# Optimization experiments

Hardware: AMD Instinct MI355X
Metric: run time of the kernel (lower is better)

## Reference

```python
import jax, jax.numpy as jnp
import numpy as np

K = 3       # kernel_size
STRIDE = 1
PAD = 1
EPS = 1e-12  # F.normalize eps


def setup_inputs() -> dict:
    key = jax.random.key(0)
    k1, k2, k3 = jax.random.split(key, 3)
    x = jax.random.normal(k1, (8, 128, 112, 112), dtype=jnp.float32)
    weight = jax.random.normal(k2, (256, 128, K, K), dtype=jnp.float32)
    bias = jax.random.normal(k3, (256,), dtype=jnp.float32)
    return {"x": x, "weight": weight, "bias": bias}


def reference(x, weight, bias):
    B, C, H, W = x.shape
    Cout = weight.shape[0]
    oh = (H + 2 * PAD - K) // STRIDE + 1
    ow = (W + 2 * PAD - K) // STRIDE + 1
    # im2col: [B, C*K*K, oh, ow]; feature order (C, kh, kw), same as torch F.unfold
    patches = jax.lax.conv_general_dilated_patches(
        x, (K, K), (STRIDE, STRIDE), [(PAD, PAD), (PAD, PAD)],
        dimension_numbers=("NCHW", "OIHW", "NCHW"))
    u = patches.reshape(B, C * K * K, oh * ow)
    # L2-normalize each patch column (dim=1), matching F.normalize(p=2, dim=1)
    norm = jnp.sqrt(jnp.sum(u * u, axis=1, keepdims=True))
    u = u / jnp.maximum(norm, EPS)
    # GEMM: [Cout, C*K*K] x [B, C*K*K, L] -> [B, Cout, L]
    out = jnp.einsum("od,bdl->bol", weight.reshape(Cout, -1), u)
    out = out.reshape(B, Cout, oh, ow) + bias[None, :, None, None]
    return out
```

## Files before the change

### kernel.cpp

```cpp
#include <hip/hip_runtime.h>

#define CIN    128
#define COUT   256
#define Hh     112
#define Ww     112
#define HW     12544
#define NBATCH 8
#define NPIX   (NBATCH*HW)
#define KD     (CIN*9)
#define PH     114
#define PPIX   (NBATCH*PH*PH)

typedef __bf16         v8bf __attribute__((ext_vector_type(8)));
typedef float          v4f  __attribute__((ext_vector_type(4)));

__device__ __forceinline__ unsigned short f2bf(float f) {
  unsigned int u = __float_as_uint(f);
  u += 0x7FFFu + ((u >> 16) & 1u);
  return (unsigned short)(u >> 16);
}

__device__ __forceinline__ void gl_lds16(const void* g, void* l) {
  __builtin_amdgcn_global_load_lds(
      (const __attribute__((address_space(1))) void*)g,
      (__attribute__((address_space(3))) void*)l, 16, 0, 0);
}

#define USS 130
__global__ __launch_bounds__(256) void k_pre(
    const float* __restrict__ x, const float* __restrict__ w,
    unsigned short* __restrict__ xbp, unsigned short* __restrict__ wpk,
    float* __restrict__ sq)
{
  __shared__ unsigned short US[112 * USS];
  __shared__ float sqp[112 * 4];

  int tid = threadIdx.x;
  int bid = blockIdx.x;

  if (bid >= NBATCH * PH) {
    int t = (bid - NBATCH * PH) * 2048 + tid * 8;
#pragma unroll
    for (int i = 0; i < 8; ++i) {
      int idx = t + i;
      int o  = idx / KD;
      int rr = idx - o * KD;
      int kk = rr >> 7;
      int c  = rr & 127;
      wpk[idx] = f2bf(w[(size_t)o * KD + c * 9 + kk]);
    }
    return;
  }

  int b  = bid / PH;
  int py = bid - b * PH;
  unsigned int* dstrow = (unsigned int*)xbp +
      (size_t)(b * PH + py) * PH * (CIN / 2);

  if (py == 0 || py == PH - 1) {
    uint4 z = {0, 0, 0, 0};
    for (int h = tid; h < PH * (CIN / 8); h += 256)
      *(uint4*)(dstrow + h * 4) = z;
    return;
  }

  int oy  = py - 1;
  int l   = tid & 63;
  int wid = tid >> 6;
  const float* xp = x + (size_t)b * CIN * HW + (size_t)oy * Ww;
  bool valid = l < 56;

  float a0 = 0.0f, a1 = 0.0f;
#pragma unroll
  for (int it = 0; it < 32; ++it) {
    int c = wid * 32 + it;
    float vx = 0.0f, vy = 0.0f;
    if (valid) {
      float2 v = *(const float2*)(xp + (size_t)c * HW + 2 * l);
      vx = v.x; vy = v.y;
    }
    a0 += vx * vx;
    a1 += vy * vy;
    if (valid) {
      US[(2 * l) * USS + c]     = f2bf(vx);
      US[(2 * l + 1) * USS + c] = f2bf(vy);
    }
  }
  if (valid) { sqp[(2 * l) * 4 + wid] = a0; sqp[(2 * l + 1) * 4 + wid] = a1; }
  __syncthreads();

  if (tid < 112) {
    float s = sqp[tid * 4] + sqp[tid * 4 + 1] + sqp[tid * 4 + 2] + sqp[tid * 4 + 3];
    sq[(size_t)b * HW + (size_t)oy * Ww + tid] = s;
  }

  unsigned int* dst = dstrow + (CIN / 2);
  for (int h = tid; h < 112 * 16; h += 256) {
    int px = h >> 4, part = h & 15;
    const unsigned short* s = &US[px * USS + part * 8];
    uint4 vv;
    vv.x = *(const unsigned int*)(s + 0);
    vv.y = *(const unsigned int*)(s + 2);
    vv.z = *(const unsigned int*)(s + 4);
    vv.w = *(const unsigned int*)(s + 6);
    *(uint4*)(dst + h * 4) = vv;
  }

  if (tid < 32) {
    uint4 z = {0, 0, 0, 0};
    int px   = (tid >> 4) ? (PH - 1) : 0;
    int part = tid & 15;
    *(uint4*)(dstrow + px * (CIN / 2) + part * 4) = z;
  }
}

__device__ __forceinline__ void conv_tile(
    unsigned short* Ab, unsigned short* Bb,
    int t, bool do_stage,
    v4f (&acc)[8][4], const int (&pb)[4],
    const unsigned short* __restrict__ asrc,
    const unsigned short* __restrict__ xbp,
    int wm, int wn, int quad, int l16, int wid)
{
#pragma unroll
  for (int h = 0; h < 2; ++h) {
    v8bf bfr[4];
    int cch = (h * 4 + quad) ^ (l16 & 7);
#pragma unroll
    for (int nt = 0; nt < 4; ++nt)
      bfr[nt] = *(const v8bf*)&Bb[(wn * 64 + nt * 16 + l16) * 64 + cch * 8];
#pragma unroll
    for (int mh = 0; mh < 2; ++mh) {
      v8bf af[4];
#pragma unroll
      for (int m2 = 0; m2 < 4; ++m2)
        af[m2] = *(const v8bf*)&Ab[(wm * 128 + (mh * 4 + m2) * 16 + l16) * 64 + cch * 8];
      __builtin_amdgcn_s_setprio(1);
#pragma unroll
      for (int m2 = 0; m2 < 4; ++m2)
#pragma unroll
        for (int nt = 0; nt < 4; ++nt)
          acc[mh * 4 + m2][nt] = __builtin_amdgcn_mfma_f32_16x16x32_bf16(
              af[m2], bfr[nt], acc[mh * 4 + m2][nt], 0, 0, 0);
      __builtin_amdgcn_s_setprio(0);
    }
  }
  __builtin_amdgcn_sched_barrier(0);
  __builtin_amdgcn_s_barrier();
  __builtin_amdgcn_sched_barrier(0);
  if (do_stage) {
    int t2 = t + 2;
    int kk = t2 >> 1;
    int kh = kk / 3, kw = kk - 3 * kh;
    int soff = (kh * PH + kw) * CIN + (t2 & 1) * 64;
#pragma unroll
    for (int jj = 0; jj < 4; ++jj)
      gl_lds16(asrc + (size_t)jj * 64 * KD + t2 * 64,
               &Ab[(jj * 64 + wid * 8) * 64]);
#pragma unroll
    for (int jj = 0; jj < 4; ++jj)
      gl_lds16(xbp + pb[jj] + soff,
               &Bb[(jj * 64 + wid * 8) * 64]);
    asm volatile("s_waitcnt vmcnt(8)" ::: "memory");
  } else {
    asm volatile("s_waitcnt vmcnt(0)" ::: "memory");
  }
  __builtin_amdgcn_sched_barrier(0);
  __builtin_amdgcn_s_barrier();
  __builtin_amdgcn_sched_barrier(0);
}

#define SLAB2 260
__global__ __launch_bounds__(512, 2) void k_conv(
    const unsigned short* __restrict__ wp,
    const unsigned short* __restrict__ xbp,
    const float* __restrict__ sq,
    const float* __restrict__ bias,
    float* __restrict__ out)
{
  extern __shared__ __align__(16) char smem[];
  unsigned short* As0 = (unsigned short*)smem;
  unsigned short* Bs0 = As0 + 256 * 64;
  unsigned short* As1 = Bs0 + 256 * 64;
  unsigned short* Bs1 = As1 + 256 * 64;
  float* slab = (float*)smem;

  int tid  = threadIdx.x;
  int lane = tid & 63;
  int wid  = tid >> 6;
  int wm   = wid >> 2;
  int wn   = wid & 3;
  int quad = lane >> 4;
  int l16  = lane & 15;

  int L  = blockIdx.x;
  int bn = (L & 7) * 49 + (L >> 3);
  int nbase = bn * 256;

  int srow = tid >> 3;
  int g16  = (tid & 7) ^ (srow & 7);

  const unsigned short* asrc = wp + (size_t)srow * KD + g16 * 8;

  int pb[4];
#pragma unroll
  for (int jj = 0; jj < 4; ++jj) {
    int n  = nbase + jj * 64 + srow;
    int b  = n / HW;  int r  = n - b * HW;
    int oy = r / Ww;  int ox = r - oy * Ww;
    pb[jj] = ((b * PH + oy) * PH + ox) * CIN + g16 * 8;
  }

  v4f acc[8][4];
#pragma unroll
  for (int mt = 0; mt < 8; ++mt)
#pragma unroll
    for (int nt = 0; nt < 4; ++nt)
#pragma unroll
      for (int q = 0; q < 4; ++q) acc[mt][nt][q] = 0.0f;

#pragma unroll
  for (int jj = 0; jj < 4; ++jj)
    gl_lds16(asrc + (size_t)jj * 64 * KD, &As0[(jj * 64 + wid * 8) * 64]);
#pragma unroll
  for (int jj = 0; jj < 4; ++jj)
    gl_lds16(xbp + pb[jj], &Bs0[(jj * 64 + wid * 8) * 64]);
#pragma unroll
  for (int jj = 0; jj < 4; ++jj)
    gl_lds16(asrc + (size_t)jj * 64 * KD + 64, &As1[(jj * 64 + wid * 8) * 64]);
#pragma unroll
  for (int jj = 0; jj < 4; ++jj)
    gl_lds16(xbp + pb[jj] + 64, &Bs1[(jj * 64 + wid * 8) * 64]);
  asm volatile("s_waitcnt vmcnt(8)" ::: "memory");
  __builtin_amdgcn_sched_barrier(0);
  __builtin_amdgcn_s_barrier();
  __builtin_amdgcn_sched_barrier(0);

  for (int i = 0; i < 8; ++i) {
    conv_tile(As0, Bs0, 2 * i,     true, acc, pb, asrc, xbp, wm, wn, quad, l16, wid);
    conv_tile(As1, Bs1, 2 * i + 1, true, acc, pb, asrc, xbp, wm, wn, quad, l16, wid);
  }
  conv_tile(As0, Bs0, 16, false, acc, pb, asrc, xbp, wm, wn, quad, l16, wid);
  conv_tile(As1, Bs1, 17, false, acc, pb, asrc, xbp, wm, wn, quad, l16, wid);

  float invv[4];
#pragma unroll
  for (int nt = 0; nt < 4; ++nt) {
    int n  = nbase + wn * 64 + nt * 16 + l16;
    int b  = n / HW;  int r  = n - b * HW;
    int oy = r / Ww;  int ox = r - oy * Ww;
    const float* s = sq + (size_t)b * HW;
    float a2 = 0.0f;
#pragma unroll
    for (int dy = -1; dy <= 1; ++dy) {
      int iy = oy + dy;
      if (iy < 0 || iy >= Hh) continue;
#pragma unroll
      for (int dx = -1; dx <= 1; ++dx) {
        int ix = ox + dx;
        if (ix < 0 || ix >= Ww) continue;
        a2 += s[iy * Ww + ix];
      }
    }
    invv[nt] = 1.0f / fmaxf(sqrtf(a2), 1e-12f);
  }

  int bb = nbase / HW;
  int rr = nbase - bb * HW;
  float* obase = out + (size_t)bb * COUT * HW + rr;

#pragma unroll
  for (int p = 0; p < 4; ++p) {
    if (p) __syncthreads();
    if (wm == (p >> 1)) {
      int base_mt = (p & 1) * 4;
#pragma unroll
      for (int m2 = 0; m2 < 4; ++m2)
#pragma unroll
        for (int nt = 0; nt < 4; ++nt) {
          int col = wn * 64 + nt * 16 + l16;
#pragma unroll
          for (int reg = 0; reg < 4; ++reg)
            slab[(m2 * 16 + quad * 4 + reg) * SLAB2 + col] =
                acc[base_mt + m2][nt][reg] * invv[nt];
        }
    }
    __syncthreads();
    int r  = tid >> 3;
    int o  = p * 64 + r;
    float bv = bias[o];
    float* orow = obase + (size_t)o * HW;
#pragma unroll
    for (int k = 0; k < 8; ++k) {
      int c4 = (tid & 7) * 4 + k * 32;
      v4f v = *(const v4f*)&slab[r * SLAB2 + c4];
      v4f r2;
#pragma unroll
      for (int q = 0; q < 4; ++q) r2[q] = v[q] + bv;
      *(v4f*)(orow + c4) = r2;
    }
  }
}

extern "C" void kernel_launch(void* const* d_in, const int* in_sizes, int n_in,
                              void* d_out, int out_size, void* d_ws, size_t ws_size,
                              hipStream_t stream) {
  const float* x    = (const float*)d_in[0];
  const float* w    = (const float*)d_in[1];
  const float* bias = (const float*)d_in[2];
  float* out        = (float*)d_out;

  char* ws = (char*)d_ws;
  unsigned short* xbp = (unsigned short*)ws;
  size_t off = (size_t)PPIX * CIN * 2;
  unsigned short* wpk = (unsigned short*)(ws + off);
  off += (size_t)COUT * KD * 2;
  float* sq = (float*)(ws + off);

  static bool attr_done = false;
  if (!attr_done) {
    hipFuncSetAttribute((const void*)k_conv,
                        hipFuncAttributeMaxDynamicSharedMemorySize, 131072);
    attr_done = true;
  }

  k_pre<<<NBATCH * PH + (COUT * KD) / 2048, 256, 0, stream>>>(x, w, xbp, wpk, sq);
  k_conv<<<392, 512, 131072, stream>>>(wpk, xbp, sq, bias, out);
}
```

Baseline: 219.2 us.

## Split conv tile into four MFMA quadrants interleaved with LDS reads and staging

Restructures the per-K-tile inner loop into four 128x... quadrant phases (HipKittens-style 8-wave ping-pong), each preceded by a partial LDS fragment load and a workgroup barrier, with the global-to-LDS prefetch issued before the last quadrant's MFMAs. The aim is to overlap LDS reads and global prefetch with matrix math and reduce register pressure from holding all fragments at once. It adds several extra s_barriers per tile, which can cost synchronization time if waves don't ping-pong well.

```diff
diff --git a/kernel.cpp b/kernel.cpp
--- a/kernel.cpp
+++ b/kernel.cpp
@@ -26,6 +26,8 @@
       (__attribute__((address_space(3))) void*)l, 16, 0, 0);
 }
 
+#define SB() __builtin_amdgcn_sched_barrier(0)
+
 #define USS 130
 __global__ __launch_bounds__(256) void k_pre(
     const float* __restrict__ x, const float* __restrict__ w,
@@ -122,32 +124,74 @@
     const unsigned short* __restrict__ xbp,
     int wm, int wn, int quad, int l16, int wid)
 {
+  v8bf afr[2][4], bf0[2][2], bf1[2][2];
+
 #pragma unroll
   for (int h = 0; h < 2; ++h) {
-    v8bf bfr[4];
     int cch = (h * 4 + quad) ^ (l16 & 7);
 #pragma unroll
-    for (int nt = 0; nt < 4; ++nt)
-      bfr[nt] = *(const v8bf*)&Bb[(wn * 64 + nt * 16 + l16) * 64 + cch * 8];
-#pragma unroll
-    for (int mh = 0; mh < 2; ++mh) {
-      v8bf af[4];
-#pragma unroll
-      for (int m2 = 0; m2 < 4; ++m2)
-        af[m2] = *(const v8bf*)&Ab[(wm * 128 + (mh * 4 + m2) * 16 + l16) * 64 + cch * 8];
-      __builtin_amdgcn_s_setprio(1);
-#pragma unroll
-      for (int m2 = 0; m2 < 4; ++m2)
-#pragma unroll
-        for (int nt = 0; nt < 4; ++nt)
-          acc[mh * 4 + m2][nt] = __builtin_amdgcn_mfma_f32_16x16x32_bf16(
-              af[m2], bfr[nt], acc[mh * 4 + m2][nt], 0, 0, 0);
-      __builtin_amdgcn_s_setprio(0);
-    }
-  }
-  __builtin_amdgcn_sched_barrier(0);
-  __builtin_amdgcn_s_barrier();
-  __builtin_amdgcn_sched_barrier(0);
+    for (int m2 = 0; m2 < 4; ++m2)
+      afr[h][m2] = *(const v8bf*)&Ab[(wm * 128 + m2 * 16 + l16) * 64 + cch * 8];
+#pragma unroll
+    for (int n2 = 0; n2 < 2; ++n2)
+      bf0[h][n2] = *(const v8bf*)&Bb[(wn * 64 + n2 * 16 + l16) * 64 + cch * 8];
+  }
+  SB(); __builtin_amdgcn_s_barrier();
+  asm volatile("s_waitcnt lgkmcnt(0)" ::: "memory"); SB();
+  __builtin_amdgcn_s_setprio(1);
+#pragma unroll
+  for (int h = 0; h < 2; ++h)
+#pragma unroll
+    for (int m2 = 0; m2 < 4; ++m2)
+#pragma unroll
+      for (int n2 = 0; n2 < 2; ++n2)
+        acc[m2][n2] = __builtin_amdgcn_mfma_f32_16x16x32_bf16(
+            afr[h][m2], bf0[h][n2], acc[m2][n2], 0, 0, 0);
+  __builtin_amdgcn_s_setprio(0);
+  SB(); __builtin_amdgcn_s_barrier(); SB();
+
+#pragma unroll
+  for (int h = 0; h < 2; ++h) {
+    int cch = (h * 4 + quad) ^ (l16 & 7);
+#pragma unroll
+    for (int n2 = 0; n2 < 2; ++n2)
+      bf1[h][n2] = *(const v8bf*)&Bb[(wn * 64 + 32 + n2 * 16 + l16) * 64 + cch * 8];
+  }
+  SB(); __builtin_amdgcn_s_barrier();
+  asm volatile("s_waitcnt lgkmcnt(0)" ::: "memory"); SB();
+  __builtin_amdgcn_s_setprio(1);
+#pragma unroll
+  for (int h = 0; h < 2; ++h)
+#pragma unroll
+    for (int m2 = 0; m2 < 4; ++m2)
+#pragma unroll
+      for (int n2 = 0; n2 < 2; ++n2)
+        acc[m2][2 + n2] = __builtin_amdgcn_mfma_f32_16x16x32_bf16(
+            afr[h][m2], bf1[h][n2], acc[m2][2 + n2], 0, 0, 0);
+  __builtin_amdgcn_s_setprio(0);
+  SB(); __builtin_amdgcn_s_barrier(); SB();
+
+#pragma unroll
+  for (int h = 0; h < 2; ++h) {
+    int cch = (h * 4 + quad) ^ (l16 & 7);
+#pragma unroll
+    for (int m2 = 0; m2 < 4; ++m2)
+      afr[h][m2] = *(const v8bf*)&Ab[(wm * 128 + 64 + m2 * 16 + l16) * 64 + cch * 8];
+  }
+  SB(); __builtin_amdgcn_s_barrier();
+  asm volatile("s_waitcnt lgkmcnt(0)" ::: "memory"); SB();
+  __builtin_amdgcn_s_setprio(1);
+#pragma unroll
+  for (int h = 0; h < 2; ++h)
+#pragma unroll
+    for (int m2 = 0; m2 < 4; ++m2)
+#pragma unroll
+      for (int n2 = 0; n2 < 2; ++n2)
+        acc[4 + m2][2 + n2] = __builtin_amdgcn_mfma_f32_16x16x32_bf16(
+            afr[h][m2], bf1[h][n2], acc[4 + m2][2 + n2], 0, 0, 0);
+  __builtin_amdgcn_s_setprio(0);
+  SB(); __builtin_amdgcn_s_barrier(); SB();
+
   if (do_stage) {
     int t2 = t + 2;
     int kk = t2 >> 1;
@@ -161,13 +205,24 @@
     for (int jj = 0; jj < 4; ++jj)
       gl_lds16(xbp + pb[jj] + soff,
                &Bb[(jj * 64 + wid * 8) * 64]);
+  }
+  __builtin_amdgcn_s_setprio(1);
+#pragma unroll
+  for (int h = 0; h < 2; ++h)
+#pragma unroll
+    for (int m2 = 0; m2 < 4; ++m2)
+#pragma unroll
+      for (int n2 = 0; n2 < 2; ++n2)
+        acc[4 + m2][n2] = __builtin_amdgcn_mfma_f32_16x16x32_bf16(
+            afr[h][m2], bf0[h][n2], acc[4 + m2][n2], 0, 0, 0);
+  __builtin_amdgcn_s_setprio(0);
+  SB();
+  if (do_stage) {
     asm volatile("s_waitcnt vmcnt(8)" ::: "memory");
   } else {
     asm volatile("s_waitcnt vmcnt(0)" ::: "memory");
   }
-  __builtin_amdgcn_sched_barrier(0);
-  __builtin_amdgcn_s_barrier();
-  __builtin_amdgcn_sched_barrier(0);
+  SB(); __builtin_amdgcn_s_barrier(); SB();
 }
 
 #define SLAB2 260
@@ -232,9 +287,7 @@
   for (int jj = 0; jj < 4; ++jj)
     gl_lds16(xbp + pb[jj] + 64, &Bs1[(jj * 64 + wid * 8) * 64]);
   asm volatile("s_waitcnt vmcnt(8)" ::: "memory");
-  __builtin_amdgcn_sched_barrier(0);
-  __builtin_amdgcn_s_barrier();
-  __builtin_amdgcn_sched_barrier(0);
+  SB(); __builtin_amdgcn_s_barrier(); SB();
 
   for (int i = 0; i < 8; ++i) {
     conv_tile(As0, Bs0, 2 * i,     true, acc, pb, asrc, xbp, wm, wn, quad, l16, wid);
```

Result: no change. 219.8 us (+0.3%).
